# Optimization experiments

Hardware: AMD Instinct MI355X
Metric: run time of the kernel (lower is better)

## Reference

```python
import jax, jax.numpy as jnp
import numpy as np


def avg_pool_2x2(x):
    # x: [B, H, W, C] -> [B, H//2, W//2, C], non-overlapping 2x2 mean (Keras AveragePooling2D default)
    B, H, W, C = x.shape
    return x.reshape(B, H // 2, 2, W // 2, 2, C).mean(axis=(2, 4))


def setup_inputs() -> dict:
    key = jax.random.key(0)
    k1, k2, k3, k4, k5 = jax.random.split(key, 5)
    B, H, W, C = 16, 64, 64, 512
    x = jax.random.normal(k1, (B, H, W, C), dtype=jnp.float32)
    Wf = jax.random.normal(k2, (C, C // 8), dtype=jnp.float32) * 0.02
    Wg = jax.random.normal(k3, (C, C // 8), dtype=jnp.float32) * 0.02
    Wh = jax.random.normal(k4, (C, C // 2), dtype=jnp.float32) * 0.02
    Wo = jax.random.normal(k5, (C // 2, C), dtype=jnp.float32) * 0.02
    return {"x": x, "Wf": Wf, "Wg": Wg, "Wh": Wh, "Wo": Wo}


def reference(x, Wf, Wg, Wh, Wo):
    B, H, W, C = x.shape
    # 1x1 convs are per-pixel matmuls over channels
    f = jnp.einsum('bhwc,cd->bhwd', x, Wf).reshape(B, H * W, C // 8)          # queries
    xp = avg_pool_2x2(x)                                                      # [B,H/2,W/2,C]
    g = jnp.einsum('bhwc,cd->bhwd', xp, Wg).reshape(B, H * W // 4, C // 8)    # keys
    h = jnp.einsum('bhwc,cd->bhwd', xp, Wh).reshape(B, H * W // 4, C // 2)    # values
    attn = jax.nn.softmax(jnp.einsum('bqd,bkd->bqk', f, g), axis=-1)          # [B, HW, HW/4]
    y = jnp.einsum('bqk,bkd->bqd', attn, h).reshape(B, H, W, C // 2)
    out = jnp.einsum('bhwd,dc->bhwc', y, Wo) + x                              # residual
    return out
```

## Files before the change

### kernel.cpp

```cpp
#include <hip/hip_runtime.h>


#define DEVI static __device__ __forceinline__

typedef float f32x4  __attribute__((ext_vector_type(4)));
typedef float f32x16 __attribute__((ext_vector_type(16)));
typedef short bf16x8 __attribute__((ext_vector_type(8)));

DEVI short f2bf(float f) {
  union { float f; unsigned u; } v; v.f = f;
  unsigned r = v.u + 0x7FFFu + ((v.u >> 16) & 1u);
  return (short)(r >> 16);
}
DEVI float b2f(short s) {
  union { unsigned u; float f; } v; v.u = ((unsigned)(unsigned short)s) << 16; return v.f;
}
DEVI unsigned pack2(float a, float b) {
  return (unsigned)(unsigned short)f2bf(a) | ((unsigned)(unsigned short)f2bf(b) << 16);
}
DEVI f32x4 mfma16(bf16x8 a, bf16x8 b, f32x4 c) {
  return __builtin_amdgcn_mfma_f32_16x16x32_bf16(a, b, c, 0, 0, 0);
}
DEVI f32x16 mfma32(bf16x8 a, bf16x8 b, f32x16 c) {
  return __builtin_amdgcn_mfma_f32_32x32x16_bf16(a, b, c, 0, 0, 0);
}
DEVI void gload16(const short* gsrc, short* lds) {
  __builtin_amdgcn_global_load_lds(
      (const __attribute__((address_space(1))) void*)gsrc,
      (__attribute__((address_space(3))) void*)lds, 16, 0, 0);
}

__global__ __launch_bounds__(256) void prep_weights(
    const float* __restrict__ Wf, const float* __restrict__ Wg,
    const float* __restrict__ Wh, const float* __restrict__ Wo,
    short* __restrict__ WfT, short* __restrict__ WgT,
    short* __restrict__ WhT, short* __restrict__ WoT) {
  int i = blockIdx.x * 256 + threadIdx.x;
  const float* src; short* dst; int K, N, e;
  if (i < 32768)       { src = Wf; dst = WfT; K = 512; N = 64;  e = i; }
  else if (i < 65536)  { src = Wg; dst = WgT; K = 512; N = 64;  e = i - 32768; }
  else if (i < 196608) { src = Wh; dst = WhT; K = 512; N = 256; e = i - 65536; }
  else                 { src = Wo; dst = WoT; K = 256; N = 512; e = i - 196608; }
  int n = e / K, k = e - n * K;
  dst[e] = f2bf(src[(long)k * N + n]);
}

template<bool SRC_F32>
DEVI void stage64(short* lds, const void* gsrc, int rows, int stride, int tid) {
  const int chunks = rows * 8;
  for (int c = tid; c < chunks; c += 256) {
    int row = c >> 3, slot = c & 7;
    int dstb = row*128 + ((slot ^ (row & 7)) << 4);
    bf16x8 v;
    if (SRC_F32) {
      const float* s = (const float*)gsrc + (long)row*stride + slot*8;
      float4 u0 = *(const float4*)s;
      float4 u1 = *(const float4*)(s + 4);
      v[0]=f2bf(u0.x); v[1]=f2bf(u0.y); v[2]=f2bf(u0.z); v[3]=f2bf(u0.w);
      v[4]=f2bf(u1.x); v[5]=f2bf(u1.y); v[6]=f2bf(u1.z); v[7]=f2bf(u1.w);
    } else {
      v = *(const bf16x8*)((const short*)gsrc + (long)row*stride + slot*8);
    }
    *(bf16x8*)((char*)lds + dstb) = v;
  }
}

template<bool A_F32, bool POOL>
__global__ __launch_bounds__(256) void gemm_k512(const void* __restrict__ A,
    const short* __restrict__ BT, short* __restrict__ C, int Nfull,
    short* __restrict__ xp) {
  __shared__ short As[128*64];
  __shared__ short Bs[64*64];
  const int m0 = blockIdx.x * 128;
  const int n0 = blockIdx.y * 64;
  const int tid = threadIdx.x, w = tid >> 6, lane = tid & 63;
  const int l15 = lane & 15, lhi = lane >> 4;
  const int wr = w >> 1, wc = w & 1;
  f32x4 acc[4][2] = {};
  for (int kt = 0; kt < 8; ++kt) {
    const int k0 = kt * 64;
    if constexpr (A_F32)
      stage64<true >(As, (const float*)A + (long)m0*512 + k0, 128, 512, tid);
    else
      stage64<false>(As, (const short*)A + (long)m0*512 + k0, 128, 512, tid);
    stage64<false>(Bs, BT + (long)n0*512 + k0, 64, 512, tid);
    __syncthreads();
    if constexpr (POOL) {
      const long pr0 = (long)(m0 >> 12)*1024 + ((m0 & 4095) >> 7)*32;
      int wp = tid >> 3, cs = tid & 7;
      const char* Ab = (const char*)As;
      bf16x8 v00 = *(const bf16x8*)(Ab + (2*wp  )*128 + ((cs ^ ((2*wp  )&7))<<4));
      bf16x8 v01 = *(const bf16x8*)(Ab + (2*wp+1)*128 + ((cs ^ ((2*wp+1)&7))<<4));
      bf16x8 v10 = *(const bf16x8*)(Ab + (64+2*wp)*128 + ((cs ^ ((2*wp  )&7))<<4));
      bf16x8 v11 = *(const bf16x8*)(Ab + (65+2*wp)*128 + ((cs ^ ((2*wp+1)&7))<<4));
      bf16x8 o;
      #pragma unroll
      for (int j = 0; j < 8; ++j)
        o[j] = f2bf(0.25f*(b2f(v00[j])+b2f(v01[j])+b2f(v10[j])+b2f(v11[j])));
      *(bf16x8*)(xp + (pr0 + wp)*512 + k0 + cs*8) = o;
    }
    bf16x8 af[4][2], bfr[2][2];
    #pragma unroll
    for (int mi = 0; mi < 4; ++mi)
      #pragma unroll
      for (int ks = 0; ks < 2; ++ks) {
        int m = wr*64 + mi*16 + l15;
        int slot = lhi + ks*4;
        af[mi][ks] = *(const bf16x8*)((const char*)As + m*128 + ((slot ^ (m & 7)) << 4));
      }
    #pragma unroll
    for (int ni = 0; ni < 2; ++ni)
      #pragma unroll
      for (int ks = 0; ks < 2; ++ks) {
        int n = wc*32 + ni*16 + l15;
        int slot = lhi + ks*4;
        bfr[ni][ks] = *(const bf16x8*)((const char*)Bs + n*128 + ((slot ^ (n & 7)) << 4));
      }
    #pragma unroll
    for (int ks = 0; ks < 2; ++ks)
      #pragma unroll
      for (int mi = 0; mi < 4; ++mi)
        #pragma unroll
        for (int ni = 0; ni < 2; ++ni)
          acc[mi][ni] = mfma16(af[mi][ks], bfr[ni][ks], acc[mi][ni]);
    __syncthreads();
  }
  #pragma unroll
  for (int mi = 0; mi < 4; ++mi)
    #pragma unroll
    for (int ni = 0; ni < 2; ++ni)
      #pragma unroll
      for (int r = 0; r < 4; ++r) {
        long row = m0 + wr*64 + mi*16 + lhi*4 + r;
        int col = n0 + wc*32 + ni*16 + l15;
        C[row * (long)Nfull + col] = f2bf(acc[mi][ni][r]);
      }
}

__global__ __launch_bounds__(256) void transpose_h(const short* __restrict__ h,
                                                   short* __restrict__ hT) {
  __shared__ short t[64][72];
  const int k0 = blockIdx.x * 64, n0 = blockIdx.y * 64, b = blockIdx.z;
  const int tid = threadIdx.x;
  {
    int row = tid >> 2, cch = (tid & 3) * 16;
    const short* src = h + ((long)b*1024 + k0 + row) * 256 + n0 + cch;
    *(bf16x8*)&t[row][cch]     = *(const bf16x8*)src;
    *(bf16x8*)&t[row][cch + 8] = *(const bf16x8*)(src + 8);
  }
  __syncthreads();
  {
    int n = tid >> 2, kch = (tid & 3) * 16;
    bf16x8 lo, hi;
    #pragma unroll
    for (int j = 0; j < 8; ++j) { lo[j] = t[kch + j][n]; hi[j] = t[kch + 8 + j][n]; }
    short* dst = hT + ((long)b*256 + n0 + n) * 1024 + k0 + kch;
    *(bf16x8*)dst       = lo;
    *(bf16x8*)(dst + 8) = hi;
  }
}

__global__ __launch_bounds__(512, 2) void attn_kernel(const short* __restrict__ f,
    const short* __restrict__ g, const short* __restrict__ hT, short* __restrict__ y) {
  extern __shared__ __align__(16) char smem[];
  const int b = blockIdx.y, q0 = blockIdx.x * 256;
  const int tid = threadIdx.x, w = tid >> 6, lane = tid & 63;
  const int l31 = lane & 31, hi = lane >> 5;

  short* Pw = (short*)(smem + 81920 + w*4096);

  bf16x8 fq[4];
  {
    const short* frow = f + ((long)b*4096 + q0 + w*32 + l31) * 64;
    #pragma unroll
    for (int ks = 0; ks < 4; ++ks) fq[ks] = *(const bf16x8*)(frow + ks*16 + hi*8);
  }

  f32x16 acc2[8] = {};
  float rsq = 0.f;

  auto stage = [&](int buf, int kt) {
    const int k0 = kt * 64;
    short* gbuf = (short*)(smem + buf*8192);
    short* hbuf = (short*)(smem + 16384 + buf*32768);
    {
      int row = (w << 3) + (lane >> 3);
      int gslot = (lane & 7) ^ (row & 7);
      gload16(g + ((long)b*1024 + k0 + row)*64 + gslot*8, gbuf + w*512);
    }
    #pragma unroll
    for (int cc = 0; cc < 4; ++cc) {
      int c = (w << 2) + cc;
      int row = (c << 3) + (lane >> 3);
      int gslot = (lane & 7) ^ (row & 7);
      gload16(hT + ((long)b*256 + row)*1024 + k0 + gslot*8, hbuf + c*512);
    }
  };

  stage(0, 0);
  __syncthreads();
  int cur = 0;
  for (int kt = 0; kt < 16; ++kt) {
    if (kt < 15) stage(cur ^ 1, kt + 1);
    const char* gcur = (const char*)(smem + cur*8192);
    const char* hcur = (const char*)(smem + 16384 + cur*32768);
    #pragma unroll
    for (int kc2 = 0; kc2 < 2; ++kc2) {
      f32x16 s2 = {};
      #pragma unroll
      for (int ks = 0; ks < 4; ++ks) {
        int key = kc2*32 + l31;
        bf16x8 gb = *(const bf16x8*)(gcur + key*128 + (((ks*2 + hi) ^ (l31 & 7)) << 4));
        s2 = mfma32(gb, fq[ks], s2);
      }
      #pragma unroll
      for (int g2 = 0; g2 < 4; ++g2) {
        float p0 = __expf(s2[g2*4+0]), p1 = __expf(s2[g2*4+1]);
        float p2 = __expf(s2[g2*4+2]), p3 = __expf(s2[g2*4+3]);
        rsq += (p0 + p1) + (p2 + p3);
        uint2 pk; pk.x = pack2(p0, p1); pk.y = pack2(p2, p3);
        int byteoff = l31*128 + ((((kc2*4 + g2) ^ (l31 & 7)) << 4) + hi*8);
        *(uint2*)((char*)Pw + byteoff) = pk;
      }
    }
    asm volatile("s_waitcnt lgkmcnt(0)" ::: "memory");
    __builtin_amdgcn_sched_barrier(0);
    __builtin_amdgcn_s_setprio(1);
    #pragma unroll
    for (int ks = 0; ks < 4; ++ks) {
      bf16x8 pa = *(const bf16x8*)((const char*)Pw + l31*128 + (((ks*2 + hi) ^ (l31 & 7)) << 4));
      #pragma unroll
      for (int nc2 = 0; nc2 < 8; ++nc2) {
        int n = nc2*32 + l31;
        bf16x8 hb = *(const bf16x8*)(hcur + n*128 + (((ks*2 + hi) ^ (l31 & 7)) << 4));
        acc2[nc2] = mfma32(hb, pa, acc2[nc2]);
      }
    }
    __builtin_amdgcn_s_setprio(0);
    __syncthreads();
    cur ^= 1;
  }
  rsq += __shfl_xor(rsq, 32);
  float ri = 1.f / rsq;
  short* yrow = y + ((long)b*4096 + q0 + w*32 + l31) * 256;
  #pragma unroll
  for (int nc2 = 0; nc2 < 8; ++nc2)
    #pragma unroll
    for (int g2 = 0; g2 < 4; ++g2) {
      short4 o;
      o.x = f2bf(acc2[nc2][g2*4+0] * ri);
      o.y = f2bf(acc2[nc2][g2*4+1] * ri);
      o.z = f2bf(acc2[nc2][g2*4+2] * ri);
      o.w = f2bf(acc2[nc2][g2*4+3] * ri);
      *(short4*)(yrow + nc2*32 + g2*8 + hi*4) = o;
    }
}

__global__ __launch_bounds__(256) void gemm_out(const short* __restrict__ y,
    const short* __restrict__ WoT, const float* __restrict__ x, float* __restrict__ out) {
  __shared__ short As[128*64];
  __shared__ short Bs[128*64];
  const int m0 = blockIdx.x * 128, n0 = blockIdx.y * 128;
  const int tid = threadIdx.x, w = tid >> 6, lane = tid & 63;
  const int l15 = lane & 15, lhi = lane >> 4;
  const int wr = w >> 1, wc = w & 1;
  f32x4 acc[4][4] = {};
  for (int kt = 0; kt < 4; ++kt) {
    const int k0 = kt * 64;
    stage64<false>(As, y   + (long)m0*256 + k0, 128, 256, tid);
    stage64<false>(Bs, WoT + (long)n0*256 + k0, 128, 256, tid);
    __syncthreads();
    bf16x8 af[4][2], bfr[4][2];
    #pragma unroll
    for (int mi = 0; mi < 4; ++mi)
      #pragma unroll
      for (int ks = 0; ks < 2; ++ks) {
        int m = wr*64 + mi*16 + l15;
        int slot = lhi + ks*4;
        af[mi][ks] = *(const bf16x8*)((const char*)As + m*128 + ((slot ^ (m & 7)) << 4));
      }
    #pragma unroll
    for (int ni = 0; ni < 4; ++ni)
      #pragma unroll
      for (int ks = 0; ks < 2; ++ks) {
        int n = wc*64 + ni*16 + l15;
        int slot = lhi + ks*4;
        bfr[ni][ks] = *(const bf16x8*)((const char*)Bs + n*128 + ((slot ^ (n & 7)) << 4));
      }
    #pragma unroll
    for (int ks = 0; ks < 2; ++ks)
      #pragma unroll
      for (int mi = 0; mi < 4; ++mi)
        #pragma unroll
        for (int ni = 0; ni < 4; ++ni)
          acc[mi][ni] = mfma16(af[mi][ks], bfr[ni][ks], acc[mi][ni]);
    __syncthreads();
  }
  #pragma unroll
  for (int mi = 0; mi < 4; ++mi)
    #pragma unroll
    for (int ni = 0; ni < 4; ++ni)
      #pragma unroll
      for (int r = 0; r < 4; ++r) {
        long row = m0 + wr*64 + mi*16 + lhi*4 + r;
        long col = n0 + wc*64 + ni*16 + l15;
        long idx = row*512 + col;
        out[idx] = acc[mi][ni][r] + x[idx];
      }
}

extern "C" void kernel_launch(void* const* d_in, const int* in_sizes, int n_in,
                              void* d_out, int out_size, void* d_ws, size_t ws_size,
                              hipStream_t stream) {
  const float* x  = (const float*)d_in[0];
  const float* Wf = (const float*)d_in[1];
  const float* Wg = (const float*)d_in[2];
  const float* Wh = (const float*)d_in[3];
  const float* Wo = (const float*)d_in[4];
  float* out = (float*)d_out;

  short* xp  = (short*)d_ws;
  short* fb  = xp  + (long)16*1024*512;
  short* gb  = fb  + (long)65536*64;
  short* hb  = gb  + (long)16384*64;
  short* hTb = hb  + (long)16384*256;
  short* yb  = hTb + (long)16*256*1024;
  short* WfT = yb  + (long)65536*256;
  short* WgT = WfT + 64*512;
  short* WhT = WgT + 64*512;
  short* WoT = WhT + 256*512;

  hipFuncSetAttribute((const void*)attn_kernel,
                      hipFuncAttributeMaxDynamicSharedMemorySize, 114688);

  prep_weights<<<1536, 256, 0, stream>>>(Wf, Wg, Wh, Wo, WfT, WgT, WhT, WoT);
  gemm_k512<true , true ><<<dim3(512, 1), 256, 0, stream>>>((const void*)x,  WfT, fb, 64,  xp);
  gemm_k512<false, false><<<dim3(128, 1), 256, 0, stream>>>((const void*)xp, WgT, gb, 64,  nullptr);
  gemm_k512<false, false><<<dim3(128, 4), 256, 0, stream>>>((const void*)xp, WhT, hb, 256, nullptr);
  transpose_h <<<dim3(16, 4, 16), 256, 0, stream>>>(hb, hTb);
  attn_kernel <<<dim3(16, 16), 512, 114688, stream>>>(fb, gb, hTb, yb);
  gemm_out    <<<dim3(512, 4), 256, 0, stream>>>(yb, WoT, x, out);
}
```

Measured before the change: 211.5 us.

## Fuse output projection and residual add into attention kernel epilogue

The attention kernel now repacks its normalized accumulators into bf16 MFMA operands in registers using permlane32 swaps. It then multiplies them by WoT (read directly from global memory) and adds the residual x before writing out. This removes the separate gemm_out launch and the bf16 y round trip through global memory. The trade-off is a longer epilogue per block: the attention grid is only 256 blocks of 512 threads, WoT is reloaded from global/L2 by every wave, and extra register pressure may hurt the main loop.

```diff
diff --git a/kernel.cpp b/kernel.cpp
--- a/kernel.cpp
+++ b/kernel.cpp
@@ -161,7 +161,9 @@
 }
 
 __global__ __launch_bounds__(512, 2) void attn_kernel(const short* __restrict__ f,
-    const short* __restrict__ g, const short* __restrict__ hT, short* __restrict__ y) {
+    const short* __restrict__ g, const short* __restrict__ hT,
+    const short* __restrict__ WoT, const float* __restrict__ x,
+    float* __restrict__ out) {
   extern __shared__ __align__(16) char smem[];
   const int b = blockIdx.y, q0 = blockIdx.x * 256;
   const int tid = threadIdx.x, w = tid >> 6, lane = tid & 63;
@@ -242,71 +244,45 @@
   }
   rsq += __shfl_xor(rsq, 32);
   float ri = 1.f / rsq;
-  short* yrow = y + ((long)b*4096 + q0 + w*32 + l31) * 256;
+  bf16x8 yB[16];
   #pragma unroll
-  for (int nc2 = 0; nc2 < 8; ++nc2)
+  for (int nc2 = 0; nc2 < 8; ++nc2) {
+    #pragma unroll
+    for (int fh = 0; fh < 2; ++fh) {
+      const int G = fh*8;
+      unsigned a0 = pack2(acc2[nc2][G+0]*ri, acc2[nc2][G+1]*ri);
+      unsigned a1 = pack2(acc2[nc2][G+2]*ri, acc2[nc2][G+3]*ri);
+      unsigned b0 = pack2(acc2[nc2][G+4]*ri, acc2[nc2][G+5]*ri);
+      unsigned b1 = pack2(acc2[nc2][G+6]*ri, acc2[nc2][G+7]*ri);
+      asm volatile("v_permlane32_swap_b32 %0, %1" : "+v"(b0), "+v"(a0));
+      asm volatile("v_permlane32_swap_b32 %0, %1" : "+v"(b1), "+v"(a1));
+      union { unsigned u[4]; bf16x8 v; } pk;
+      pk.u[0] = a0; pk.u[1] = a1; pk.u[2] = b0; pk.u[3] = b1;
+      yB[nc2*2 + fh] = pk.v;
+    }
+  }
+  const long qrow = (long)b*4096 + q0 + w*32 + l31;
+  const float* xrow = x + qrow*512;
+  float* orow = out + qrow*512;
+  for (int cc2 = 0; cc2 < 16; ++cc2) {
+    f32x16 ao = {};
+    #pragma unroll
+    for (int ns = 0; ns < 16; ++ns) {
+      bf16x8 wo = *(const bf16x8*)(WoT + (cc2*32 + l31)*256 + ns*16 + hi*8);
+      ao = mfma32(wo, yB[ns], ao);
+    }
     #pragma unroll
     for (int g2 = 0; g2 < 4; ++g2) {
-      short4 o;
-      o.x = f2bf(acc2[nc2][g2*4+0] * ri);
-      o.y = f2bf(acc2[nc2][g2*4+1] * ri);
-      o.z = f2bf(acc2[nc2][g2*4+2] * ri);
-      o.w = f2bf(acc2[nc2][g2*4+3] * ri);
-      *(short4*)(yrow + nc2*32 + g2*8 + hi*4) = o;
-    }
-}
-
-__global__ __launch_bounds__(256) void gemm_out(const short* __restrict__ y,
-    const short* __restrict__ WoT, const float* __restrict__ x, float* __restrict__ out) {
-  __shared__ short As[128*64];
-  __shared__ short Bs[128*64];
-  const int m0 = blockIdx.x * 128, n0 = blockIdx.y * 128;
-  const int tid = threadIdx.x, w = tid >> 6, lane = tid & 63;
-  const int l15 = lane & 15, lhi = lane >> 4;
-  const int wr = w >> 1, wc = w & 1;
-  f32x4 acc[4][4] = {};
-  for (int kt = 0; kt < 4; ++kt) {
-    const int k0 = kt * 64;
-    stage64<false>(As, y   + (long)m0*256 + k0, 128, 256, tid);
-    stage64<false>(Bs, WoT + (long)n0*256 + k0, 128, 256, tid);
-    __syncthreads();
-    bf16x8 af[4][2], bfr[4][2];
-    #pragma unroll
-    for (int mi = 0; mi < 4; ++mi)
-      #pragma unroll
-      for (int ks = 0; ks < 2; ++ks) {
-        int m = wr*64 + mi*16 + l15;
-        int slot = lhi + ks*4;
-        af[mi][ks] = *(const bf16x8*)((const char*)As + m*128 + ((slot ^ (m & 7)) << 4));
-      }
-    #pragma unroll
-    for (int ni = 0; ni < 4; ++ni)
-      #pragma unroll
-      for (int ks = 0; ks < 2; ++ks) {
-        int n = wc*64 + ni*16 + l15;
-        int slot = lhi + ks*4;
-        bfr[ni][ks] = *(const bf16x8*)((const char*)Bs + n*128 + ((slot ^ (n & 7)) << 4));
-      }
-    #pragma unroll
-    for (int ks = 0; ks < 2; ++ks)
-      #pragma unroll
-      for (int mi = 0; mi < 4; ++mi)
-        #pragma unroll
-        for (int ni = 0; ni < 4; ++ni)
-          acc[mi][ni] = mfma16(af[mi][ks], bfr[ni][ks], acc[mi][ni]);
-    __syncthreads();
-  }
-  #pragma unroll
-  for (int mi = 0; mi < 4; ++mi)
-    #pragma unroll
-    for (int ni = 0; ni < 4; ++ni)
-      #pragma unroll
-      for (int r = 0; r < 4; ++r) {
-        long row = m0 + wr*64 + mi*16 + lhi*4 + r;
-        long col = n0 + wc*64 + ni*16 + l15;
-        long idx = row*512 + col;
-        out[idx] = acc[mi][ni][r] + x[idx];
-      }
+      int c = cc2*32 + g2*8 + hi*4;
+      float4 xv = *(const float4*)(xrow + c);
+      float4 ov;
+      ov.x = ao[g2*4+0] + xv.x;
+      ov.y = ao[g2*4+1] + xv.y;
+      ov.z = ao[g2*4+2] + xv.z;
+      ov.w = ao[g2*4+3] + xv.w;
+      *(float4*)(orow + c) = ov;
+    }
+  }
 }
 
 extern "C" void kernel_launch(void* const* d_in, const int* in_sizes, int n_in,
@@ -324,8 +300,7 @@
   short* gb  = fb  + (long)65536*64;
   short* hb  = gb  + (long)16384*64;
   short* hTb = hb  + (long)16384*256;
-  short* yb  = hTb + (long)16*256*1024;
-  short* WfT = yb  + (long)65536*256;
+  short* WfT = hTb + (long)16*256*1024;
   short* WgT = WfT + 64*512;
   short* WhT = WgT + 64*512;
   short* WoT = WhT + 256*512;
@@ -338,6 +313,5 @@
   gemm_k512<false, false><<<dim3(128, 1), 256, 0, stream>>>((const void*)xp, WgT, gb, 64,  nullptr);
   gemm_k512<false, false><<<dim3(128, 4), 256, 0, stream>>>((const void*)xp, WhT, hb, 256, nullptr);
   transpose_h <<<dim3(16, 4, 16), 256, 0, stream>>>(hb, hTb);
-  attn_kernel <<<dim3(16, 16), 512, 114688, stream>>>(fb, gb, hTb, yb);
-  gemm_out    <<<dim3(512, 4), 256, 0, stream>>>(yb, WoT, x, out);
-}
+  attn_kernel <<<dim3(16, 16), 512, 114688, stream>>>(fb, gb, hTb, WoT, x, out);
+}
```

After: 207.8 us. Within noise of the previous version (-1.7%).
